# Optimization experiments

Measured on AMD Instinct MI355X. Metric: run time of the kernel, lower is better.

The kernel has to match this reference:

```python
import jax, jax.numpy as jnp
import numpy as np

EPS = 1e-5  # BatchNorm eps (inference mode: running_mean=0, running_var=1)


def _bn(x, gamma, beta):
    # eval-mode BatchNorm1d over channel dim of (B, C, N)
    scale = gamma / jnp.sqrt(1.0 + EPS)
    return x * scale[None, :, None] + beta[None, :, None]


def setup_inputs() -> dict:
    key = jax.random.key(0)
    ks = jax.random.split(key, 9)
    B, C, N = 16, 512, 4096
    h, k, u, m = 4, 16, 4, 7
    v = 512 // h  # dim_v = out_channels // nhead = 128
    x = jax.random.normal(ks[0], (B, C, N), jnp.float32)
    Wq = jax.random.normal(ks[1], (k * h, C), jnp.float32) * 0.05
    gq = 1.0 + 0.1 * jax.random.normal(ks[2], (k * h,), jnp.float32)
    bq = 0.1 * jax.random.normal(ks[3], (k * h,), jnp.float32)
    Wk = jax.random.normal(ks[4], (k * u, C), jnp.float32) * 0.05
    Wv = jax.random.normal(ks[5], (v * u, C), jnp.float32) * 0.05
    gv = 1.0 + 0.1 * jax.random.normal(ks[6], (v * u,), jnp.float32)
    bv = 0.1 * jax.random.normal(ks[7], (v * u,), jnp.float32)
    emb = jax.random.normal(ks[8], (k, u, 1, m), jnp.float32)  # Conv2d weight (O,I,1,m)
    return {"x": x, "Wq": Wq, "gq": gq, "bq": bq, "Wk": Wk,
            "Wv": Wv, "gv": gv, "bv": bv, "emb": emb}


def reference(x, Wq, gq, bq, Wk, Wv, gv, bv, emb):
    B, C, N = x.shape
    k, u, _, m = emb.shape
    h = Wq.shape[0] // k
    v = Wv.shape[0] // u
    pad = (m - 1) // 2
    # 1x1 conv projections == channel matmuls
    queries = _bn(jnp.einsum('oc,bcn->bon', Wq, x), gq, bq).reshape(B, h, k, N)
    keys = jax.nn.softmax(
        jnp.einsum('oc,bcn->bon', Wk, x).reshape(B, k, u, N), axis=-1)
    values = _bn(jnp.einsum('oc,bcn->bon', Wv, x), gv, bv).reshape(B, v, u, N)
    # content lambda: (B, k, v)
    lambda_c = jnp.einsum('bkun,bvun->bkv', keys, values)
    y_c = jnp.einsum('bhkn,bkv->bhvn', queries, lambda_c)
    # position lambda via conv2d over reinterpreted values (B, u, v, N)
    values_2d = values.reshape(B, u, v, N)
    lambda_p = jax.lax.conv_general_dilated(
        values_2d, emb, window_strides=(1, 1),
        padding=[(0, 0), (pad, pad)],
        dimension_numbers=('NCHW', 'OIHW', 'NCHW'))  # (B, k, v, N)
    y_p = jnp.einsum('bhkn,bkvn->bhvn', queries, lambda_p)
    return (y_c + y_p).reshape(B, h * v, N)
```

## Files before the change

kernel.cpp:

```cpp
#include <hip/hip_runtime.h>
#include <hip/hip_bf16.h>


#define B_  16
#define C_  512
#define N_  4096
#define OT  640

typedef __bf16 bf16x8 __attribute__((ext_vector_type(8)));
typedef float  f32x4  __attribute__((ext_vector_type(4)));

static constexpr size_t PROJ_ELEMS = (size_t)B_ * 128 * N_;
static constexpr size_t VBF_OFF    = PROJ_ELEMS;
static constexpr size_t KBF_OFF    = VBF_OFF + ((size_t)B_ * 512 * N_) / 2;
static constexpr size_t XT_OFF     = KBF_OFF + ((size_t)B_ * 64 * N_) / 2;
static constexpr size_t WB_OFF     = XT_OFF + ((size_t)B_ * N_ * C_) / 2;
static constexpr size_t SB_OFF     = WB_OFF + ((size_t)OT * C_) / 2;
static constexpr size_t LAM_OFF    = SB_OFF + (size_t)OT * 2;

__device__ __forceinline__ void load_lds16(const void* g, void* l) {
  __builtin_amdgcn_global_load_lds(
      (const __attribute__((address_space(1))) void*)g,
      (__attribute__((address_space(3))) void*)l, 16, 0, 0);
}

__device__ __forceinline__ unsigned short f2bf(float f) {
  __hip_bfloat16 h = __float2bfloat16(f);
  return *(unsigned short*)&h;
}

__global__ __launch_bounds__(256) void pack_kernel(
    const float* __restrict__ Wq, const float* __restrict__ gq, const float* __restrict__ bq,
    const float* __restrict__ Wk, const float* __restrict__ Wv,
    const float* __restrict__ gv, const float* __restrict__ bv,
    __hip_bfloat16* __restrict__ Wall, float* __restrict__ sb) {
  int idx = blockIdx.x * 256 + threadIdx.x;
  if (idx < OT * C_) {
    int row = idx >> 9;
    float val;
    if (row < 64)        val = Wq[idx];
    else if (row < 128)  val = Wk[idx - 64 * C_];
    else                 val = Wv[idx - 128 * C_];
    Wall[idx] = __float2bfloat16(val);
  }
  if (idx < OT) {
    const float inv = 0.99999500003749971875f;
    float s, bi;
    if (idx < 64)       { s = gq[idx] * inv;       bi = bq[idx]; }
    else if (idx < 128) { s = 1.0f;                bi = 0.0f; }
    else                { s = gv[idx - 128] * inv; bi = bv[idx - 128]; }
    sb[idx * 2]     = s;
    sb[idx * 2 + 1] = bi;
  }
}

__global__ __launch_bounds__(256) void convert_x(
    const float* __restrict__ x, __hip_bfloat16* __restrict__ xT) {
  const int n0 = blockIdx.x * 64;
  const int c0 = blockIdx.y * 64;
  const int b  = blockIdx.z;
  __shared__ float tile[64][65];
  const int t = threadIdx.x;
  const int tr = t >> 4, tc4 = (t & 15) * 4;
  const float* xb = x + ((size_t)b * C_ + c0) * N_ + n0;
#pragma unroll
  for (int i = 0; i < 4; ++i) {
    float4 v = *(const float4*)&xb[(size_t)(i * 16 + tr) * N_ + tc4];
    *(float4*)&tile[i * 16 + tr][tc4] = v;
  }
  __syncthreads();
  __hip_bfloat16* ob = xT + ((size_t)b * N_ + n0) * C_ + c0;
#pragma unroll
  for (int i = 0; i < 4; ++i) {
    int rn = i * 16 + tr;
    uint2 pk;
    __hip_bfloat16* ph = (__hip_bfloat16*)&pk;
#pragma unroll
    for (int j = 0; j < 4; ++j) ph[j] = __float2bfloat16(tile[tc4 + j][rn]);
    *(uint2*)&ob[(size_t)rn * C_ + tc4] = pk;
  }
}

__global__ __launch_bounds__(256) void gemm_mfma(
    const __hip_bfloat16* __restrict__ xT, const __hip_bfloat16* __restrict__ Wb,
    const float* __restrict__ sb, float* __restrict__ proj,
    __hip_bfloat16* __restrict__ vbf) {
  const int t = threadIdx.x;
  const int l = t & 63, w = t >> 6;
  const int wr = w >> 1, wc = w & 1;
  const int m0 = blockIdx.y * 128, n0 = blockIdx.x * 128;
  const int b = blockIdx.z;
  const __hip_bfloat16* xb = xT + (size_t)b * N_ * C_;

  __shared__ __hip_bfloat16 Als[128 * 32];
  __shared__ __hip_bfloat16 Bls[128 * 32];

  const int srow = w * 16 + (l >> 2);
  const int scol = (l & 3) * 8;
  const __hip_bfloat16* gA = Wb + (size_t)(m0 + srow) * C_ + scol;
  const __hip_bfloat16* gB = xb + (size_t)(n0 + srow) * C_ + scol;
  __hip_bfloat16* lA = &Als[w * 512 + l * 8];
  __hip_bfloat16* lB = &Bls[w * 512 + l * 8];

  const int fr = l & 15;
  const int kg = (l >> 4) * 8;

  f32x4 acc[4][4] = {};

  for (int c0 = 0; c0 < C_; c0 += 32) {
    __syncthreads();
#pragma unroll
    for (int i = 0; i < 2; ++i) {
      load_lds16(gA + (size_t)i * 64 * C_ + c0, lA + i * 2048);
      load_lds16(gB + (size_t)i * 64 * C_ + c0, lB + i * 2048);
    }
    __syncthreads();
    bf16x8 af[4], bfr[4];
#pragma unroll
    for (int m = 0; m < 4; ++m)
      af[m] = *(const bf16x8*)&Als[(size_t)(wr * 64 + m * 16 + fr) * 32 + kg];
#pragma unroll
    for (int n = 0; n < 4; ++n)
      bfr[n] = *(const bf16x8*)&Bls[(size_t)(wc * 64 + n * 16 + fr) * 32 + kg];
#pragma unroll
    for (int m = 0; m < 4; ++m)
#pragma unroll
      for (int n = 0; n < 4; ++n)
        acc[m][n] = __builtin_amdgcn_mfma_f32_16x16x32_bf16(af[m], bfr[n], acc[m][n], 0, 0, 0);
  }

  float* pb = proj + (size_t)b * 128 * N_;
  __hip_bfloat16* vb = vbf + (size_t)b * 512 * N_;
  const int rb = (l >> 4) * 4;
#pragma unroll
  for (int m = 0; m < 4; ++m) {
#pragma unroll
    for (int r = 0; r < 4; ++r) {
      int grow = m0 + wr * 64 + m * 16 + rb + r;
      float s = sb[grow * 2], bi = sb[grow * 2 + 1];
      if (grow < 128) {
#pragma unroll
        for (int n = 0; n < 4; ++n) {
          int gcol = n0 + wc * 64 + n * 16 + fr;
          pb[(size_t)grow * N_ + gcol] = acc[m][n][r] * s + bi;
        }
      } else {
#pragma unroll
        for (int n = 0; n < 4; ++n) {
          int gcol = n0 + wc * 64 + n * 16 + fr;
          vb[(size_t)(grow - 128) * N_ + gcol] = __float2bfloat16(acc[m][n][r] * s + bi);
        }
      }
    }
  }
}

__global__ __launch_bounds__(256) void softmax_keys(
    const float* __restrict__ proj, __hip_bfloat16* __restrict__ kbf) {
  const int r = blockIdx.x, b = blockIdx.y;
  const float* row = proj + ((size_t)b * 128 + 64 + r) * N_;
  __hip_bfloat16* orow = kbf + ((size_t)b * 64 + r) * N_;
  const int t = threadIdx.x;
  float4 v[4];
  float mx = -1e30f;
#pragma unroll
  for (int i = 0; i < 4; ++i) {
    v[i] = ((const float4*)row)[t + i * 256];
    mx = fmaxf(mx, fmaxf(fmaxf(v[i].x, v[i].y), fmaxf(v[i].z, v[i].w)));
  }
  __shared__ float red[4];
#pragma unroll
  for (int off = 32; off; off >>= 1) mx = fmaxf(mx, __shfl_xor(mx, off));
  if ((t & 63) == 0) red[t >> 6] = mx;
  __syncthreads();
  mx = fmaxf(fmaxf(red[0], red[1]), fmaxf(red[2], red[3]));
  float sum = 0.f;
#pragma unroll
  for (int i = 0; i < 4; ++i) {
    v[i].x = __expf(v[i].x - mx);
    v[i].y = __expf(v[i].y - mx);
    v[i].z = __expf(v[i].z - mx);
    v[i].w = __expf(v[i].w - mx);
    sum += v[i].x + v[i].y + v[i].z + v[i].w;
  }
  __syncthreads();
#pragma unroll
  for (int off = 32; off; off >>= 1) sum += __shfl_xor(sum, off);
  if ((t & 63) == 0) red[t >> 6] = sum;
  __syncthreads();
  float invs = 1.0f / (red[0] + red[1] + red[2] + red[3]);
#pragma unroll
  for (int i = 0; i < 4; ++i) {
    uint2 pk;
    pk.x = f2bf(v[i].x * invs) | ((unsigned)f2bf(v[i].y * invs) << 16);
    pk.y = f2bf(v[i].z * invs) | ((unsigned)f2bf(v[i].w * invs) << 16);
    ((uint2*)orow)[t + i * 256] = pk;
  }
}

__global__ __launch_bounds__(256) void lambda_c_kernel(
    const __hip_bfloat16* __restrict__ kbf, const __hip_bfloat16* __restrict__ vbf,
    float* __restrict__ lam) {
  const int ns = blockIdx.x;
  const int b  = blockIdx.y >> 1;
  const int vh = blockIdx.y & 1;
  const int nb = ns * 128;
  const int t = threadIdx.x, l = t & 63, w = t >> 6;
  __shared__ __hip_bfloat16 klds[64 * 128];

  const __hip_bfloat16* kg = kbf + (size_t)b * 64 * N_ + nb;
#pragma unroll
  for (int i = 0; i < 4; ++i) {
    int task = i * 256 + t;
    int row = task >> 4, gc = task & 15;
    uint4 val = *(const uint4*)&kg[(size_t)row * N_ + gc * 8];
    int byte = (row * 256 + gc * 16) ^ (((row >> 2) & 7) << 4);
    *(uint4*)((char*)klds + byte) = val;
  }
  __syncthreads();

  const int fr = l & 15, g = l >> 4;
  const int vv0 = (vh * 4 + w) * 16;
  const __hip_bfloat16* vg = vbf + (size_t)b * 512 * N_ + nb;
  f32x4 acc = {};
#pragma unroll
  for (int ui = 0; ui < 4; ++ui) {
#pragma unroll
    for (int s = 0; s < 4; ++s) {
      const int krow = fr * 4 + ui;
      const int byte = (krow * 256 + s * 64 + g * 16) ^ (((krow >> 2) & 7) << 4);
      bf16x8 af = *(const bf16x8*)((const char*)klds + byte);
      const int vrow = (vv0 + fr) * 4 + ui;
      bf16x8 bf = *(const bf16x8*)&vg[(size_t)vrow * N_ + s * 32 + g * 8];
      acc = __builtin_amdgcn_mfma_f32_16x16x32_bf16(af, bf, acc, 0, 0, 0);
    }
  }
  float* lamb = lam + (size_t)b * 16 * 128;
#pragma unroll
  for (int r = 0; r < 4; ++r)
    atomicAdd(&lamb[(g * 4 + r) * 128 + vv0 + fr], acc[r]);
}

__global__ __launch_bounds__(256) void final_kernel(
    const float* __restrict__ proj, const __hip_bfloat16* __restrict__ vbf,
    const float* __restrict__ lam, const float* __restrict__ emb,
    float* __restrict__ out) {
  const int n0  = blockIdx.x * 32;
  const int vq  = blockIdx.y;
  const int b   = blockIdx.z;
  const int vv0 = vq * 32;
  const float* pb = proj + (size_t)b * 128 * N_;
  const __hip_bfloat16* vb = vbf + (size_t)b * 512 * N_;
  const int t = threadIdx.x, l = t & 63, w = t >> 6;

  __shared__ __hip_bfloat16 P_lds[32][40][4];
  __shared__ float lamT[32][16];

  const int fr = l & 15;
  const int g  = l >> 4;
  const int rb = g * 4;
  const int gb0 = g & 1, gb1 = g >> 1;

  union { uint4 u; bf16x8 v; } ef;
  {
    unsigned short eh[8];
#pragma unroll
    for (int j = 0; j < 8; ++j) {
      int kap = g * 8 + j;
      float val = 0.f;
      if (kap < 28) val = emb[fr * 28 + (kap & 3) * 7 + (kap >> 2)];
      eh[j] = f2bf(val);
    }
    ef.u.x = eh[0] | ((unsigned)eh[1] << 16);
    ef.u.y = eh[2] | ((unsigned)eh[3] << 16);
    ef.u.z = eh[4] | ((unsigned)eh[5] << 16);
    ef.u.w = eh[6] | ((unsigned)eh[7] << 16);
  }

  float qreg[4][4][2];
#pragma unroll
  for (int hh = 0; hh < 4; ++hh)
#pragma unroll
    for (int r = 0; r < 4; ++r)
#pragma unroll
      for (int nt = 0; nt < 2; ++nt)
        qreg[hh][r][nt] = pb[(size_t)(hh * 16 + rb + r) * N_ + n0 + nt * 16 + fr];

#pragma unroll
  for (int i = 0; i < 5; ++i) {
    int task = i * 256 + t;
    int vl = task / 40;
    int np = task - vl * 40;
    int gn = n0 + np - 3;
    unsigned short hv[4];
    if (np < 38 && gn >= 0 && gn < N_) {
#pragma unroll
      for (int ui = 0; ui < 4; ++ui)
        hv[ui] = *(const unsigned short*)&vb[(size_t)(ui * 128 + vv0 + vl) * N_ + gn];
    } else {
      hv[0] = hv[1] = hv[2] = hv[3] = 0;
    }
    uint2 pk;
    pk.x = hv[0] | ((unsigned)hv[1] << 16);
    pk.y = hv[2] | ((unsigned)hv[3] << 16);
    *(uint2*)&P_lds[vl][np][0] = pk;
  }
  {
    int kk = t >> 5, vl = t & 31;
    lamT[vl][kk]     = lam[((size_t)b * 16 + kk) * 128 + vv0 + vl];
    lamT[vl][kk + 8] = lam[((size_t)b * 16 + kk + 8) * 128 + vv0 + vl];
  }
  __syncthreads();

  float* obase = out + ((size_t)b * 512 + g * 128 + vv0) * N_ + n0;
#pragma unroll
  for (int mi = 0; mi < 16; ++mi) {
    const int vl_t = w * 8 + (mi >> 1);
    const int nt   = mi & 1;
    const int nlc  = nt * 16 + fr;
    union { uint4 u; bf16x8 v; } bf;
    {
      const uint2 lo = *(const uint2*)&P_lds[vl_t][nlc + 2 * g][0];
      const uint2 hi = *(const uint2*)&P_lds[vl_t][nlc + 2 * g + 1][0];
      bf.u.x = lo.x; bf.u.y = lo.y; bf.u.z = hi.x; bf.u.w = hi.y;
    }
    f32x4 c = *(const f32x4*)&lamT[vl_t][rb];
    f32x4 d = __builtin_amdgcn_mfma_f32_16x16x32_bf16(ef.v, bf.v, c, 0, 0, 0);
    float p0 = qreg[0][0][nt] * d[0] + qreg[0][1][nt] * d[1] + qreg[0][2][nt] * d[2] + qreg[0][3][nt] * d[3];
    float p1 = qreg[1][0][nt] * d[0] + qreg[1][1][nt] * d[1] + qreg[1][2][nt] * d[2] + qreg[1][3][nt] * d[3];
    float p2 = qreg[2][0][nt] * d[0] + qreg[2][1][nt] * d[1] + qreg[2][2][nt] * d[2] + qreg[2][3][nt] * d[3];
    float p3 = qreg[3][0][nt] * d[0] + qreg[3][1][nt] * d[1] + qreg[3][2][nt] * d[2] + qreg[3][3][nt] * d[3];
    float e0 = gb0 ? p0 : p1;
    float e1 = gb0 ? p2 : p3;
    float s0 = (gb0 ? p1 : p0) + __shfl_xor(e0, 16);
    float s1 = (gb0 ? p3 : p2) + __shfl_xor(e1, 16);
    float e2 = gb1 ? s0 : s1;
    float yv = (gb1 ? s1 : s0) + __shfl_xor(e2, 32);
    obase[(size_t)vl_t * N_ + nlc] = yv;
  }
}

extern "C" void kernel_launch(void* const* d_in, const int* in_sizes, int n_in,
                              void* d_out, int out_size, void* d_ws, size_t ws_size,
                              hipStream_t stream) {
  const float* x   = (const float*)d_in[0];
  const float* Wq  = (const float*)d_in[1];
  const float* gq  = (const float*)d_in[2];
  const float* bq  = (const float*)d_in[3];
  const float* Wk  = (const float*)d_in[4];
  const float* Wv  = (const float*)d_in[5];
  const float* gv  = (const float*)d_in[6];
  const float* bv  = (const float*)d_in[7];
  const float* emb = (const float*)d_in[8];

  float* ws   = (float*)d_ws;
  float* proj = ws;
  __hip_bfloat16* vbf   = (__hip_bfloat16*)(ws + VBF_OFF);
  __hip_bfloat16* kbf   = (__hip_bfloat16*)(ws + KBF_OFF);
  __hip_bfloat16* xTb   = (__hip_bfloat16*)(ws + XT_OFF);
  __hip_bfloat16* Wallb = (__hip_bfloat16*)(ws + WB_OFF);
  float* sb   = ws + SB_OFF;
  float* lam  = ws + LAM_OFF;
  float* out  = (float*)d_out;

  hipMemsetAsync(lam, 0, (size_t)B_ * 16 * 128 * sizeof(float), stream);
  pack_kernel<<<dim3(1280), 256, 0, stream>>>(Wq, gq, bq, Wk, Wv, gv, bv, Wallb, sb);
  convert_x<<<dim3(N_ / 64, C_ / 64, B_), 256, 0, stream>>>(x, xTb);
  gemm_mfma<<<dim3(N_ / 128, OT / 128, B_), 256, 0, stream>>>(xTb, Wallb, sb, proj, vbf);
  softmax_keys<<<dim3(64, B_), 256, 0, stream>>>(proj, kbf);
  lambda_c_kernel<<<dim3(32, 32), 256, 0, stream>>>(kbf, vbf, lam);
  final_kernel<<<dim3(N_ / 32, 4, B_), 256, 0, stream>>>(proj, vbf, lam, emb, out);
}
```

Before: 211.5 us.

## Store all projections as bf16 and fold softmax normalization into lambda kernel

The GEMM now writes queries, keys and values all as bf16 into one buffer instead of fp32 queries/keys plus a separate bf16 value buffer. The softmax pass only computes per-row max and inverse sum, and the lambda_c kernel applies exp and normalization while staging keys into LDS, so the normalized key tensor is never materialized. Lambda_c also covers both value halves per block, which halves the grid and reuses the keys loaded into LDS. This cuts global memory traffic, at the cost of lower precision for queries and pre-softmax logits.

```diff
diff --git a/kernel.cpp b/kernel.cpp
--- a/kernel.cpp
+++ b/kernel.cpp
@@ -10,13 +10,12 @@
 typedef __bf16 bf16x8 __attribute__((ext_vector_type(8)));
 typedef float  f32x4  __attribute__((ext_vector_type(4)));
 
-static constexpr size_t PROJ_ELEMS = (size_t)B_ * 128 * N_;
-static constexpr size_t VBF_OFF    = PROJ_ELEMS;
-static constexpr size_t KBF_OFF    = VBF_OFF + ((size_t)B_ * 512 * N_) / 2;
-static constexpr size_t XT_OFF     = KBF_OFF + ((size_t)B_ * 64 * N_) / 2;
-static constexpr size_t WB_OFF     = XT_OFF + ((size_t)B_ * N_ * C_) / 2;
-static constexpr size_t SB_OFF     = WB_OFF + ((size_t)OT * C_) / 2;
-static constexpr size_t LAM_OFF    = SB_OFF + (size_t)OT * 2;
+static constexpr size_t PBF_OFF = 0;
+static constexpr size_t XT_OFF  = ((size_t)B_ * OT * N_) / 2;
+static constexpr size_t WB_OFF  = XT_OFF + ((size_t)B_ * N_ * C_) / 2;
+static constexpr size_t SB_OFF  = WB_OFF + ((size_t)OT * C_) / 2;
+static constexpr size_t ST_OFF  = SB_OFF + (size_t)OT * 2;
+static constexpr size_t LAM_OFF = ST_OFF + (size_t)B_ * 64 * 2;
 
 __device__ __forceinline__ void load_lds16(const void* g, void* l) {
   __builtin_amdgcn_global_load_lds(
@@ -27,6 +26,9 @@
 __device__ __forceinline__ unsigned short f2bf(float f) {
   __hip_bfloat16 h = __float2bfloat16(f);
   return *(unsigned short*)&h;
+}
+__device__ __forceinline__ float bf2f(unsigned short u) {
+  union { unsigned int i; float f; } c; c.i = ((unsigned int)u) << 16; return c.f;
 }
 
 __global__ __launch_bounds__(256) void pack_kernel(
@@ -83,8 +85,7 @@
 
 __global__ __launch_bounds__(256) void gemm_mfma(
     const __hip_bfloat16* __restrict__ xT, const __hip_bfloat16* __restrict__ Wb,
-    const float* __restrict__ sb, float* __restrict__ proj,
-    __hip_bfloat16* __restrict__ vbf) {
+    const float* __restrict__ sb, __hip_bfloat16* __restrict__ pbf) {
   const int t = threadIdx.x;
   const int l = t & 63, w = t >> 6;
   const int wr = w >> 1, wc = w & 1;
@@ -129,8 +130,7 @@
         acc[m][n] = __builtin_amdgcn_mfma_f32_16x16x32_bf16(af[m], bfr[n], acc[m][n], 0, 0, 0);
   }
 
-  float* pb = proj + (size_t)b * 128 * N_;
-  __hip_bfloat16* vb = vbf + (size_t)b * 512 * N_;
+  __hip_bfloat16* pb = pbf + (size_t)b * OT * N_;
   const int rb = (l >> 4) * 4;
 #pragma unroll
   for (int m = 0; m < 4; ++m) {
@@ -138,36 +138,32 @@
     for (int r = 0; r < 4; ++r) {
       int grow = m0 + wr * 64 + m * 16 + rb + r;
       float s = sb[grow * 2], bi = sb[grow * 2 + 1];
-      if (grow < 128) {
-#pragma unroll
-        for (int n = 0; n < 4; ++n) {
-          int gcol = n0 + wc * 64 + n * 16 + fr;
-          pb[(size_t)grow * N_ + gcol] = acc[m][n][r] * s + bi;
-        }
-      } else {
-#pragma unroll
-        for (int n = 0; n < 4; ++n) {
-          int gcol = n0 + wc * 64 + n * 16 + fr;
-          vb[(size_t)(grow - 128) * N_ + gcol] = __float2bfloat16(acc[m][n][r] * s + bi);
-        }
+#pragma unroll
+      for (int n = 0; n < 4; ++n) {
+        int gcol = n0 + wc * 64 + n * 16 + fr;
+        pb[(size_t)grow * N_ + gcol] = __float2bfloat16(acc[m][n][r] * s + bi);
       }
     }
   }
 }
 
-__global__ __launch_bounds__(256) void softmax_keys(
-    const float* __restrict__ proj, __hip_bfloat16* __restrict__ kbf) {
+__global__ __launch_bounds__(256) void softmax_stats(
+    const __hip_bfloat16* __restrict__ pbf, float* __restrict__ stats) {
   const int r = blockIdx.x, b = blockIdx.y;
-  const float* row = proj + ((size_t)b * 128 + 64 + r) * N_;
-  __hip_bfloat16* orow = kbf + ((size_t)b * 64 + r) * N_;
+  const __hip_bfloat16* row = pbf + ((size_t)b * OT + 64 + r) * N_;
   const int t = threadIdx.x;
-  float4 v[4];
+  float f[16];
+  {
+    uint4 v1 = ((const uint4*)row)[t];
+    uint4 v2 = ((const uint4*)row)[t + 256];
+    const unsigned short* h1 = (const unsigned short*)&v1;
+    const unsigned short* h2 = (const unsigned short*)&v2;
+#pragma unroll
+    for (int j = 0; j < 8; ++j) { f[j] = bf2f(h1[j]); f[j + 8] = bf2f(h2[j]); }
+  }
   float mx = -1e30f;
 #pragma unroll
-  for (int i = 0; i < 4; ++i) {
-    v[i] = ((const float4*)row)[t + i * 256];
-    mx = fmaxf(mx, fmaxf(fmaxf(v[i].x, v[i].y), fmaxf(v[i].z, v[i].w)));
-  }
+  for (int j = 0; j < 16; ++j) mx = fmaxf(mx, f[j]);
   __shared__ float red[4];
 #pragma unroll
   for (int off = 32; off; off >>= 1) mx = fmaxf(mx, __shfl_xor(mx, off));
@@ -176,81 +172,79 @@
   mx = fmaxf(fmaxf(red[0], red[1]), fmaxf(red[2], red[3]));
   float sum = 0.f;
 #pragma unroll
-  for (int i = 0; i < 4; ++i) {
-    v[i].x = __expf(v[i].x - mx);
-    v[i].y = __expf(v[i].y - mx);
-    v[i].z = __expf(v[i].z - mx);
-    v[i].w = __expf(v[i].w - mx);
-    sum += v[i].x + v[i].y + v[i].z + v[i].w;
-  }
+  for (int j = 0; j < 16; ++j) sum += __expf(f[j] - mx);
   __syncthreads();
 #pragma unroll
   for (int off = 32; off; off >>= 1) sum += __shfl_xor(sum, off);
   if ((t & 63) == 0) red[t >> 6] = sum;
   __syncthreads();
-  float invs = 1.0f / (red[0] + red[1] + red[2] + red[3]);
-#pragma unroll
-  for (int i = 0; i < 4; ++i) {
-    uint2 pk;
-    pk.x = f2bf(v[i].x * invs) | ((unsigned)f2bf(v[i].y * invs) << 16);
-    pk.y = f2bf(v[i].z * invs) | ((unsigned)f2bf(v[i].w * invs) << 16);
-    ((uint2*)orow)[t + i * 256] = pk;
+  if (t == 0) {
+    float s = red[0] + red[1] + red[2] + red[3];
+    stats[((size_t)b * 64 + r) * 2]     = mx;
+    stats[((size_t)b * 64 + r) * 2 + 1] = 1.0f / s;
   }
 }
 
 __global__ __launch_bounds__(256) void lambda_c_kernel(
-    const __hip_bfloat16* __restrict__ kbf, const __hip_bfloat16* __restrict__ vbf,
+    const __hip_bfloat16* __restrict__ pbf, const float* __restrict__ stats,
     float* __restrict__ lam) {
   const int ns = blockIdx.x;
-  const int b  = blockIdx.y >> 1;
-  const int vh = blockIdx.y & 1;
+  const int b  = blockIdx.y;
   const int nb = ns * 128;
   const int t = threadIdx.x, l = t & 63, w = t >> 6;
   __shared__ __hip_bfloat16 klds[64 * 128];
 
-  const __hip_bfloat16* kg = kbf + (size_t)b * 64 * N_ + nb;
+  const __hip_bfloat16* kg = pbf + ((size_t)b * OT + 64) * N_ + nb;
+  const float* stb = stats + (size_t)b * 64 * 2;
 #pragma unroll
   for (int i = 0; i < 4; ++i) {
     int task = i * 256 + t;
     int row = task >> 4, gc = task & 15;
     uint4 val = *(const uint4*)&kg[(size_t)row * N_ + gc * 8];
+    float mx = stb[row * 2], ivs = stb[row * 2 + 1];
+    unsigned short* hs = (unsigned short*)&val;
+#pragma unroll
+    for (int j = 0; j < 8; ++j)
+      hs[j] = f2bf(__expf(bf2f(hs[j]) - mx) * ivs);
     int byte = (row * 256 + gc * 16) ^ (((row >> 2) & 7) << 4);
     *(uint4*)((char*)klds + byte) = val;
   }
   __syncthreads();
 
   const int fr = l & 15, g = l >> 4;
-  const int vv0 = (vh * 4 + w) * 16;
-  const __hip_bfloat16* vg = vbf + (size_t)b * 512 * N_ + nb;
-  f32x4 acc = {};
-#pragma unroll
-  for (int ui = 0; ui < 4; ++ui) {
-#pragma unroll
-    for (int s = 0; s < 4; ++s) {
-      const int krow = fr * 4 + ui;
-      const int byte = (krow * 256 + s * 64 + g * 16) ^ (((krow >> 2) & 7) << 4);
-      bf16x8 af = *(const bf16x8*)((const char*)klds + byte);
-      const int vrow = (vv0 + fr) * 4 + ui;
-      bf16x8 bf = *(const bf16x8*)&vg[(size_t)vrow * N_ + s * 32 + g * 8];
-      acc = __builtin_amdgcn_mfma_f32_16x16x32_bf16(af, bf, acc, 0, 0, 0);
-    }
-  }
+  const __hip_bfloat16* vg = pbf + ((size_t)b * OT + 128) * N_ + nb;
   float* lamb = lam + (size_t)b * 16 * 128;
 #pragma unroll
-  for (int r = 0; r < 4; ++r)
-    atomicAdd(&lamb[(g * 4 + r) * 128 + vv0 + fr], acc[r]);
+  for (int vt = 0; vt < 2; ++vt) {
+    const int vv0 = (vt * 4 + w) * 16;
+    f32x4 acc = {};
+#pragma unroll
+    for (int ui = 0; ui < 4; ++ui) {
+#pragma unroll
+      for (int s = 0; s < 4; ++s) {
+        const int krow = fr * 4 + ui;
+        const int byte = (krow * 256 + s * 64 + g * 16) ^ (((krow >> 2) & 7) << 4);
+        bf16x8 af = *(const bf16x8*)((const char*)klds + byte);
+        const int vrow = (vv0 + fr) * 4 + ui;
+        bf16x8 bf = *(const bf16x8*)&vg[(size_t)vrow * N_ + s * 32 + g * 8];
+        acc = __builtin_amdgcn_mfma_f32_16x16x32_bf16(af, bf, acc, 0, 0, 0);
+      }
+    }
+#pragma unroll
+    for (int r = 0; r < 4; ++r)
+      atomicAdd(&lamb[(g * 4 + r) * 128 + vv0 + fr], acc[r]);
+  }
 }
 
 __global__ __launch_bounds__(256) void final_kernel(
-    const float* __restrict__ proj, const __hip_bfloat16* __restrict__ vbf,
-    const float* __restrict__ lam, const float* __restrict__ emb,
-    float* __restrict__ out) {
+    const __hip_bfloat16* __restrict__ pbf, const float* __restrict__ lam,
+    const float* __restrict__ emb, float* __restrict__ out) {
   const int n0  = blockIdx.x * 32;
   const int vq  = blockIdx.y;
   const int b   = blockIdx.z;
   const int vv0 = vq * 32;
-  const float* pb = proj + (size_t)b * 128 * N_;
-  const __hip_bfloat16* vb = vbf + (size_t)b * 512 * N_;
+  const __hip_bfloat16* qb = pbf + (size_t)b * OT * N_;
+  const __hip_bfloat16* vb = pbf + ((size_t)b * OT + 128) * N_;
   const int t = threadIdx.x, l = t & 63, w = t >> 6;
 
   __shared__ __hip_bfloat16 P_lds[32][40][4];
@@ -284,7 +278,8 @@
     for (int r = 0; r < 4; ++r)
 #pragma unroll
       for (int nt = 0; nt < 2; ++nt)
-        qreg[hh][r][nt] = pb[(size_t)(hh * 16 + rb + r) * N_ + n0 + nt * 16 + fr];
+        qreg[hh][r][nt] = bf2f(*(const unsigned short*)
+            &qb[(size_t)(hh * 16 + rb + r) * N_ + n0 + nt * 16 + fr]);
 
 #pragma unroll
   for (int i = 0; i < 5; ++i) {
@@ -353,21 +348,20 @@
   const float* bv  = (const float*)d_in[7];
   const float* emb = (const float*)d_in[8];
 
-  float* ws   = (float*)d_ws;
-  float* proj = ws;
-  __hip_bfloat16* vbf   = (__hip_bfloat16*)(ws + VBF_OFF);
-  __hip_bfloat16* kbf   = (__hip_bfloat16*)(ws + KBF_OFF);
+  float* ws = (float*)d_ws;
+  __hip_bfloat16* pbf   = (__hip_bfloat16*)(ws + PBF_OFF);
   __hip_bfloat16* xTb   = (__hip_bfloat16*)(ws + XT_OFF);
   __hip_bfloat16* Wallb = (__hip_bfloat16*)(ws + WB_OFF);
-  float* sb   = ws + SB_OFF;
-  float* lam  = ws + LAM_OFF;
-  float* out  = (float*)d_out;
+  float* sb    = ws + SB_OFF;
+  float* stats = ws + ST_OFF;
+  float* lam   = ws + LAM_OFF;
+  float* out   = (float*)d_out;
 
   hipMemsetAsync(lam, 0, (size_t)B_ * 16 * 128 * sizeof(float), stream);
   pack_kernel<<<dim3(1280), 256, 0, stream>>>(Wq, gq, bq, Wk, Wv, gv, bv, Wallb, sb);
   convert_x<<<dim3(N_ / 64, C_ / 64, B_), 256, 0, stream>>>(x, xTb);
-  gemm_mfma<<<dim3(N_ / 128, OT / 128, B_), 256, 0, stream>>>(xTb, Wallb, sb, proj, vbf);
-  softmax_keys<<<dim3(64, B_), 256, 0, stream>>>(proj, kbf);
-  lambda_c_kernel<<<dim3(32, 32), 256, 0, stream>>>(kbf, vbf, lam);
-  final_kernel<<<dim3(N_ / 32, 4, B_), 256, 0, stream>>>(proj, vbf, lam, emb, out);
-}
+  gemm_mfma<<<dim3(N_ / 128, OT / 128, B_), 256, 0, stream>>>(xTb, Wallb, sb, pbf);
+  softmax_stats<<<dim3(64, B_), 256, 0, stream>>>(pbf, stats);
+  lambda_c_kernel<<<dim3(32, 16), 256, 0, stream>>>(pbf, stats, lam);
+  final_kernel<<<dim3(N_ / 32, 4, B_), 256, 0, stream>>>(pbf, lam, emb, out);
+}
```

Result: faster. 202.2 us (-4.4%).
